# Optimization experiments

Measured on AMD Instinct MI355X. Metric: run time of the kernel, lower is better.

Reference implementation:

```python
import jax, jax.numpy as jnp
import numpy as np

D_MODEL = 1024
PATCH = 16
HID = 256
VOCAB = 256

def setup_inputs() -> dict:
    key = jax.random.key(0)
    ks = jax.random.split(key, 12)
    B, N = 16, 512
    s = lambda *sh: 1.0 / np.sqrt(sh[-1])
    inp = {
        'latents': jax.random.normal(ks[0], (B, N, D_MODEL), dtype=jnp.float32),
        'target_bytes': jax.random.randint(ks[1], (B, N * PATCH), 0, VOCAB, dtype=jnp.int64),
        'W_proj': jax.random.normal(ks[2], (HID, D_MODEL), dtype=jnp.float32) * s(HID, D_MODEL),
        'b_proj': jnp.zeros((HID,), dtype=jnp.float32),
        'emb_table': jax.random.normal(ks[3], (VOCAB, HID), dtype=jnp.float32),
        'W_ih': jax.random.normal(ks[4], (3 * HID, 2 * HID), dtype=jnp.float32) * s(1, 2 * HID),
        'W_hh': jax.random.normal(ks[5], (3 * HID, HID), dtype=jnp.float32) * s(1, HID),
        'b_ih': jnp.zeros((3 * HID,), dtype=jnp.float32),
        'b_hh': jnp.zeros((3 * HID,), dtype=jnp.float32),
        'W_head': jax.random.normal(ks[6], (VOCAB, HID), dtype=jnp.float32) * s(VOCAB, HID),
        'b_head': jnp.zeros((VOCAB,), dtype=jnp.float32),
    }
    return inp

def _gru_scan(x_proj, W_hh, b_hh, h0):
    # x_proj: [T, BN, 3H] precomputed input projections (incl. b_ih)
    def step(h, xg):
        hg = h @ W_hh.T + b_hh                      # [BN, 3H]
        xr, xz, xn = jnp.split(xg, 3, axis=-1)
        hr, hz, hn = jnp.split(hg, 3, axis=-1)
        r = jax.nn.sigmoid(xr + hr)
        z = jax.nn.sigmoid(xz + hz)
        n = jnp.tanh(xn + r * hn)
        h_new = (1.0 - z) * n + z * h
        return h_new, h_new
    _, outs = jax.lax.scan(step, h0, x_proj)
    return outs                                      # [T, BN, H]

def reference(latents, target_bytes, W_proj, b_proj, emb_table, W_ih, W_hh, b_ih, b_hh, W_head, b_head):
    B, N, D = latents.shape
    BN = B * N
    latent_ctx = (latents.reshape(BN, D) @ W_proj.T + b_proj)        # [BN, H]
    targets = target_bytes.reshape(BN, PATCH)
    sos = jnp.zeros((BN, 1), dtype=targets.dtype)
    rnn_in_bytes = jnp.concatenate([sos, targets[:, :-1]], axis=1)   # [BN, P]
    emb = emb_table[rnn_in_bytes]                                    # [BN, P, H]
    lat_exp = jnp.broadcast_to(latent_ctx[:, None, :], (BN, PATCH, HID))
    rnn_input = jnp.concatenate([emb, lat_exp], axis=-1)             # [BN, P, 2H]
    x_proj = jnp.einsum('bpi,gi->bpg', rnn_input, W_ih) + b_ih       # [BN, P, 3H]
    h0 = jnp.zeros((BN, HID), dtype=latents.dtype)
    outs = _gru_scan(jnp.swapaxes(x_proj, 0, 1), W_hh, b_hh, h0)     # [P, BN, H]
    outs = jnp.swapaxes(outs, 0, 1)                                  # [BN, P, H]
    logits = jnp.einsum('bph,vh->bpv', outs, W_head) + b_head        # [BN, P, 256]
    return logits.reshape(B, N, PATCH, VOCAB)
```

## Files before the change

kernel.cpp:

```cpp
#include <hip/hip_runtime.h>
#include <math.h>

#define NSEQ 8192
#define PATCHL 16
#define HIDN 256
#define VOCABN 256

typedef __attribute__((ext_vector_type(4))) float f32x4;
typedef __attribute__((ext_vector_type(8))) short bf16x8;

__device__ __forceinline__ unsigned short f2bf(float f) {
    unsigned int x = __float_as_uint(f);
    unsigned int r = (x + 0x7fffu + ((x >> 16) & 1u)) >> 16;
    return (unsigned short)r;
}
__device__ __forceinline__ float bf2f(unsigned short b) {
    return __uint_as_float(((unsigned int)b) << 16);
}
__device__ __forceinline__ float sigf(float x)   { return 1.f / (1.f + __expf(-x)); }
__device__ __forceinline__ float tanhf_(float x) { return 2.f / (1.f + __expf(-2.f * x)) - 1.f; }

__global__ __launch_bounds__(256)
void pack_frag(const float* __restrict__ src, int ld, int col0, int nks,
               unsigned short* __restrict__ dst)
{
    const int g = blockIdx.x * 256 + threadIdx.x;
    const int lane = g & 63;
    const int ks = (g / 64) % nks;
    const int T  = g / (64 * nks);
    const float* s = src + (size_t)(T * 16 + (lane & 15)) * ld + col0 + ks * 32 + ((lane >> 4) & 3) * 8;
    unsigned int q[4];
#pragma unroll
    for (int j = 0; j < 4; j++) {
        unsigned int lo = f2bf(s[2 * j]);
        unsigned int hi = f2bf(s[2 * j + 1]);
        q[j] = lo | (hi << 16);
    }
    uint4 v; v.x = q[0]; v.y = q[1]; v.z = q[2]; v.w = q[3];
    *(uint4*)(dst + (size_t)g * 8) = v;
}

template<bool ASRC_BF16, bool OUT_BF16>
__global__ __launch_bounds__(512)
void gemm_mfma(const void* __restrict__ Asrc, int lda,
               const unsigned short* __restrict__ bpack, int nks_total,
               const float* __restrict__ bias, void* __restrict__ Cdst, int ldc,
               int K)
{
    const int tid = threadIdx.x;
    const int w = tid >> 6, lane = tid & 63;
    const int l15 = lane & 15, kg = (lane >> 4) & 3;
    const int bm = blockIdx.x * 128, bn = blockIdx.y * 64;

    __shared__ unsigned short As[2][128 * 64];

    const int srow = tid >> 2;
    const int scol = (tid & 3) * 16;
    const int nkt = K / 64;

    f32x4 acc[4];
#pragma unroll
    for (int nt = 0; nt < 4; nt++) acc[nt] = 0.f;

    const int wb0 = srow * 128 + ((scol * 2) ^ ((srow & 7) << 4));
    const int wb1 = srow * 128 + ((scol * 2 + 16) ^ ((srow & 7) << 4));

#define STAGE(kt, buf) do {                                                         \
        const int gk = (kt) * 64 + scol;                                            \
        unsigned short tmp[16];                                                     \
        if (ASRC_BF16) {                                                            \
            const unsigned short* A = (const unsigned short*)Asrc;                  \
            *(uint4*)(tmp)     = *(const uint4*)(A + (size_t)(bm + srow) * lda + gk);      \
            *(uint4*)(tmp + 8) = *(const uint4*)(A + (size_t)(bm + srow) * lda + gk + 8);  \
        } else {                                                                    \
            const float* A = (const float*)Asrc;                                    \
            const float4 a0 = *(const float4*)(A + (size_t)(bm + srow) * lda + gk);       \
            const float4 a1 = *(const float4*)(A + (size_t)(bm + srow) * lda + gk + 4);   \
            const float4 a2 = *(const float4*)(A + (size_t)(bm + srow) * lda + gk + 8);   \
            const float4 a3 = *(const float4*)(A + (size_t)(bm + srow) * lda + gk + 12);  \
            tmp[0] = f2bf(a0.x);  tmp[1] = f2bf(a0.y);  tmp[2] = f2bf(a0.z);  tmp[3] = f2bf(a0.w);   \
            tmp[4] = f2bf(a1.x);  tmp[5] = f2bf(a1.y);  tmp[6] = f2bf(a1.z);  tmp[7] = f2bf(a1.w);   \
            tmp[8] = f2bf(a2.x);  tmp[9] = f2bf(a2.y);  tmp[10] = f2bf(a2.z); tmp[11] = f2bf(a2.w);  \
            tmp[12] = f2bf(a3.x); tmp[13] = f2bf(a3.y); tmp[14] = f2bf(a3.z); tmp[15] = f2bf(a3.w);  \
        }                                                                           \
        *(uint4*)((char*)As[buf] + wb0) = *(uint4*)tmp;                             \
        *(uint4*)((char*)As[buf] + wb1) = *(uint4*)(tmp + 8);                       \
    } while (0)

    STAGE(0, 0);
    __syncthreads();

    for (int kt = 0; kt < nkt; ++kt) {
        if (kt + 1 < nkt) STAGE(kt + 1, (kt + 1) & 1);
        const unsigned short* buf = As[kt & 1];
        const int row = w * 16 + l15;
#pragma unroll
        for (int ks = 0; ks < 2; ++ks) {
            const int bo = row * 128 + (((ks * 64) + kg * 16) ^ ((row & 7) << 4));
            const bf16x8 a = *(const bf16x8*)((const char*)buf + bo);
#pragma unroll
            for (int nt = 0; nt < 4; ++nt) {
                const int T = blockIdx.y * 4 + nt;
                const bf16x8 b = *(const bf16x8*)(bpack + (((size_t)T * nks_total + (kt * 2 + ks)) * 64 + lane) * 8);
                acc[nt] = __builtin_amdgcn_mfma_f32_16x16x32_bf16(a, b, acc[nt], 0, 0, 0);
            }
        }
        __syncthreads();
    }
#undef STAGE

#pragma unroll
    for (int nt = 0; nt < 4; ++nt) {
        const int n = bn + nt * 16 + l15;
        const float bv = bias ? bias[n] : 0.f;
#pragma unroll
        for (int rr = 0; rr < 4; ++rr) {
            const int m = bm + w * 16 + kg * 4 + rr;
            const float v = acc[nt][rr] + bv;
            if (OUT_BF16) ((unsigned short*)Cdst)[(size_t)m * ldc + n] = f2bf(v);
            else          ((float*)Cdst)[(size_t)m * ldc + n] = v;
        }
    }
}

#define PMS 776
__global__ __launch_bounds__(512)
void gru_scan_fused(const int* __restrict__ bytes,
                    const float* __restrict__ latg,
                    const unsigned short* __restrict__ premixB,
                    const unsigned short* __restrict__ wpack,
                    const float* __restrict__ b_hh,
                    unsigned short* __restrict__ hh,
                    int seq0)
{
    const int tid  = threadIdx.x;
    const int w    = tid >> 6;
    const int lane = tid & 63;
    const int l15  = lane & 15;
    const int kg   = (lane >> 4) & 3;
    const int s0l  = blockIdx.x * 32;
    const int s0g  = seq0 + s0l;

    __shared__ unsigned short PMs[32 * PMS];
    __shared__ unsigned short H[32 * 256];
    __shared__ int BYs[512];

    BYs[tid] = bytes[(size_t)s0g * PATCHL + tid];

    float bhr[2], bhz[2], bhn[2];
#pragma unroll
    for (int nt = 0; nt < 2; nt++) {
        const int u = w * 32 + nt * 16 + l15;
        bhr[nt] = b_hh[u]; bhz[nt] = b_hh[256 + u]; bhn[nt] = b_hh[512 + u];
    }

    float lgr[2][2][4], lgz[2][2][4], lgn[2][2][4];
#pragma unroll
    for (int mt = 0; mt < 2; mt++)
#pragma unroll
        for (int nt = 0; nt < 2; nt++) {
            const int u = w * 32 + nt * 16 + l15;
#pragma unroll
            for (int rr = 0; rr < 4; rr++) {
                const int sg = s0g + mt * 16 + kg * 4 + rr;
                const float* lg = latg + (size_t)sg * 768;
                lgr[mt][nt][rr] = lg[u]       + bhr[nt];
                lgz[mt][nt][rr] = lg[u + 256] + bhz[nt];
                lgn[mt][nt][rr] = lg[u + 512];
            }
        }

    float hreg[2][2][4];
#pragma unroll
    for (int mt = 0; mt < 2; mt++)
#pragma unroll
        for (int nt = 0; nt < 2; nt++)
#pragma unroll
            for (int rr = 0; rr < 4; rr++) hreg[mt][nt][rr] = 0.f;

    __syncthreads();

    for (int p = 0; p < PATCHL; ++p) {
#pragma unroll
        for (int j = 0; j < 6; ++j) {
            const int idx = j * 512 + tid;
            const int row = idx / 96, col = idx - row * 96;
            const int bv = p ? BYs[row * PATCHL + p - 1] : 0;
            *(uint4*)(PMs + row * PMS + col * 8) =
                *(const uint4*)(premixB + (size_t)bv * 768 + col * 8);
        }

        if (p) {
#pragma unroll
            for (int rj = 0; rj < 4; ++rj) {
                const int row = w * 4 + rj;
                const int boff = (lane * 8) ^ ((row & 7) << 4);
                const ushort4 v = *(const ushort4*)((const char*)(H + row * 256) + boff);
                *(ushort4*)(hh + ((size_t)(s0l + row) * PATCHL + (p - 1)) * 256 + lane * 4) = v;
            }
        }

        f32x4 accr[2][2], accz[2][2], accn[2][2];
#pragma unroll
        for (int mt = 0; mt < 2; mt++)
#pragma unroll
            for (int nt = 0; nt < 2; nt++) {
                accr[mt][nt] = 0.f; accz[mt][nt] = 0.f; accn[mt][nt] = 0.f;
            }
        if (p != 0) {
#pragma unroll
            for (int ks = 0; ks < 8; ++ks) {
                bf16x8 a[2];
#pragma unroll
                for (int mt = 0; mt < 2; mt++) {
                    const int s = mt * 16 + l15;
                    const int off = (ks * 64 + kg * 16) ^ ((s & 7) << 4);
                    a[mt] = *(const bf16x8*)(H + s * 256 + (off >> 1));
                }
#pragma unroll
                for (int nt = 0; nt < 2; nt++) {
                    const int tb = w * 2 + nt;
                    const bf16x8 br = *(const bf16x8*)(wpack + (((size_t)(tb)      * 8 + ks) * 64 + lane) * 8);
                    const bf16x8 bz = *(const bf16x8*)(wpack + (((size_t)(16 + tb) * 8 + ks) * 64 + lane) * 8);
                    const bf16x8 bn = *(const bf16x8*)(wpack + (((size_t)(32 + tb) * 8 + ks) * 64 + lane) * 8);
#pragma unroll
                    for (int mt = 0; mt < 2; mt++) {
                        accr[mt][nt] = __builtin_amdgcn_mfma_f32_16x16x32_bf16(a[mt], br, accr[mt][nt], 0, 0, 0);
                        accz[mt][nt] = __builtin_amdgcn_mfma_f32_16x16x32_bf16(a[mt], bz, accz[mt][nt], 0, 0, 0);
                        accn[mt][nt] = __builtin_amdgcn_mfma_f32_16x16x32_bf16(a[mt], bn, accn[mt][nt], 0, 0, 0);
                    }
                }
            }
        }
        __syncthreads();

#pragma unroll
        for (int mt = 0; mt < 2; mt++)
#pragma unroll
            for (int nt = 0; nt < 2; nt++) {
                const int u = w * 32 + nt * 16 + l15;
#pragma unroll
                for (int rr = 0; rr < 4; rr++) {
                    const int sl = mt * 16 + kg * 4 + rr;
                    const float xr = lgr[mt][nt][rr] + bf2f(PMs[sl * PMS + u]);
                    const float xz = lgz[mt][nt][rr] + bf2f(PMs[sl * PMS + 256 + u]);
                    const float xn = lgn[mt][nt][rr] + bf2f(PMs[sl * PMS + 512 + u]);
                    const float r = sigf(xr + accr[mt][nt][rr]);
                    const float z = sigf(xz + accz[mt][nt][rr]);
                    const float n = tanhf_(xn + r * (accn[mt][nt][rr] + bhn[nt]));
                    const float hn_ = (1.f - z) * n + z * hreg[mt][nt][rr];
                    hreg[mt][nt][rr] = hn_;
                    const int bo = (2 * u) ^ ((sl & 7) << 4);
                    H[sl * 256 + (bo >> 1)] = f2bf(hn_);
                }
            }
        __syncthreads();
    }

#pragma unroll
    for (int rj = 0; rj < 4; ++rj) {
        const int row = w * 4 + rj;
        const int boff = (lane * 8) ^ ((row & 7) << 4);
        const ushort4 v = *(const ushort4*)((const char*)(H + row * 256) + boff);
        *(ushort4*)(hh + ((size_t)(s0l + row) * PATCHL + (PATCHL - 1)) * 256 + lane * 4) = v;
    }
}

extern "C" void kernel_launch(void* const* d_in, const int* in_sizes, int n_in,
                              void* d_out, int out_size, void* d_ws, size_t ws_size,
                              hipStream_t stream)
{
    const float* latents = (const float*)d_in[0];
    const int*   tb      = (const int*)d_in[1];
    const float* W_proj  = (const float*)d_in[2];
    const float* b_proj  = (const float*)d_in[3];
    const float* emb     = (const float*)d_in[4];
    const float* W_ih    = (const float*)d_in[5];
    const float* W_hh    = (const float*)d_in[6];
    const float* b_ih    = (const float*)d_in[7];
    const float* b_hh    = (const float*)d_in[8];
    const float* W_head  = (const float*)d_in[9];
    const float* b_head  = (const float*)d_in[10];
    float* out = (float*)d_out;

    char* w = (char*)d_ws;
    float* latg = (float*)w;                               w += (size_t)NSEQ * 768 * 4;
    unsigned short* ctxb    = (unsigned short*)w;          w += (size_t)NSEQ * HIDN * 2;
    unsigned short* premixB = (unsigned short*)w;          w += 256 * 768 * 2;
    unsigned short* bpack1  = (unsigned short*)w;          w += 16 * 32 * 64 * 8 * 2;
    unsigned short* bpack2  = (unsigned short*)w;          w += 48 * 8 * 64 * 8 * 2;
    unsigned short* bpack3  = (unsigned short*)w;          w += 48 * 8 * 64 * 8 * 2;
    unsigned short* wpackG  = (unsigned short*)w;          w += 48 * 8 * 64 * 8 * 2;
    unsigned short* bpackH  = (unsigned short*)w;          w += 16 * 8 * 64 * 8 * 2;
    unsigned short* hh_c    = (unsigned short*)w;
    const size_t fixed_bytes = (size_t)(w - (char*)d_ws);
    const size_t chunk_full  = (size_t)NSEQ * PATCHL * 256 * 2;

    int nch = 1;
    while (nch < 16 && fixed_bytes + chunk_full / nch > ws_size) nch <<= 1;
    const int SPC = NSEQ / nch;

    hipLaunchKernelGGL(pack_frag, dim3(128), dim3(256), 0, stream, W_proj, 1024, 0, 32, bpack1);
    hipLaunchKernelGGL(pack_frag, dim3(96),  dim3(256), 0, stream, W_ih,   512, 256, 8, bpack2);
    hipLaunchKernelGGL(pack_frag, dim3(96),  dim3(256), 0, stream, W_ih,   512, 0,   8, bpack3);
    hipLaunchKernelGGL(pack_frag, dim3(96),  dim3(256), 0, stream, W_hh,   256, 0,   8, wpackG);
    hipLaunchKernelGGL(pack_frag, dim3(32),  dim3(256), 0, stream, W_head, 256, 0,   8, bpackH);

    hipLaunchKernelGGL((gemm_mfma<false, true>), dim3(2, 12), dim3(512), 0, stream,
                       emb, 256, bpack3, 8, nullptr, premixB, 768, 256);
    hipLaunchKernelGGL((gemm_mfma<false, true>), dim3(NSEQ / 128, 4), dim3(512), 0, stream,
                       latents, 1024, bpack1, 32, b_proj, ctxb, 256, 1024);
    hipLaunchKernelGGL((gemm_mfma<true, false>), dim3(NSEQ / 128, 12), dim3(512), 0, stream,
                       ctxb, 256, bpack2, 8, b_ih, latg, 768, 256);

    for (int c = 0; c < nch; ++c) {
        const int seq0 = c * SPC;
        hipLaunchKernelGGL(gru_scan_fused, dim3(SPC / 32), dim3(512), 0, stream,
                           tb, latg, premixB, wpackG, b_hh, hh_c, seq0);
        hipLaunchKernelGGL((gemm_mfma<true, false>), dim3(SPC * PATCHL / 128, 4), dim3(512), 0, stream,
                           hh_c, 256, bpackH, 8, b_head,
                           out + (size_t)seq0 * PATCHL * VOCABN, 256, 256);
    }
}
```

Before: 409.1 us.

## Interleave gate projections as bf16 quads and stage latent gates in LDS

The latent-gate projection is now stored as bf16 in a gate-interleaved layout (r,z,n,pad per hidden unit) instead of fp32 planar. The byte-embedding premix table uses the same layout. The scan kernel stages each block's latent gates into shared memory once and reads both tables with a single 8-byte load per unit, instead of holding 24 fp32 values per thread in registers. This cuts register pressure and the global bytes for latg, but adds about 66KB of LDS per block, which may lower occupancy. It also adds bf16 rounding of the latent gates and a padded fourth slot.

```diff
diff --git a/kernel.cpp b/kernel.cpp
--- a/kernel.cpp
+++ b/kernel.cpp
@@ -40,7 +40,7 @@
     *(uint4*)(dst + (size_t)g * 8) = v;
 }
 
-template<bool ASRC_BF16, bool OUT_BF16>
+template<bool ASRC_BF16, int OUT_MODE>
 __global__ __launch_bounds__(512)
 void gemm_mfma(const void* __restrict__ Asrc, int lda,
                const unsigned short* __restrict__ bpack, int nks_total,
@@ -117,17 +117,18 @@
         for (int rr = 0; rr < 4; ++rr) {
             const int m = bm + w * 16 + kg * 4 + rr;
             const float v = acc[nt][rr] + bv;
-            if (OUT_BF16) ((unsigned short*)Cdst)[(size_t)m * ldc + n] = f2bf(v);
-            else          ((float*)Cdst)[(size_t)m * ldc + n] = v;
-        }
-    }
-}
-
-#define PMS 776
+            if (OUT_MODE == 0)      ((float*)Cdst)[(size_t)m * ldc + n] = v;
+            else if (OUT_MODE == 1) ((unsigned short*)Cdst)[(size_t)m * ldc + n] = f2bf(v);
+            else                    ((unsigned short*)Cdst)[(size_t)m * 1024 + (n & 255) * 4 + (n >> 8)] = f2bf(v);
+        }
+    }
+}
+
+#define G4S 1032
 __global__ __launch_bounds__(512)
 void gru_scan_fused(const int* __restrict__ bytes,
-                    const float* __restrict__ latg,
-                    const unsigned short* __restrict__ premixB,
+                    const unsigned short* __restrict__ latg4,
+                    const unsigned short* __restrict__ pmx4,
                     const unsigned short* __restrict__ wpack,
                     const float* __restrict__ b_hh,
                     unsigned short* __restrict__ hh,
@@ -141,11 +142,20 @@
     const int s0l  = blockIdx.x * 32;
     const int s0g  = seq0 + s0l;
 
-    __shared__ unsigned short PMs[32 * PMS];
+    __shared__ unsigned short PMs[32 * G4S];
+    __shared__ unsigned short LG[32 * G4S];
     __shared__ unsigned short H[32 * 256];
     __shared__ int BYs[512];
 
     BYs[tid] = bytes[(size_t)s0g * PATCHL + tid];
+
+#pragma unroll
+    for (int j = 0; j < 8; ++j) {
+        const int idx = j * 512 + tid;
+        const int row = idx >> 7, col = idx & 127;
+        *(uint4*)(LG + row * G4S + col * 8) =
+            *(const uint4*)(latg4 + (size_t)(s0g + row) * 1024 + col * 8);
+    }
 
     float bhr[2], bhz[2], bhn[2];
 #pragma unroll
@@ -154,26 +164,10 @@
         bhr[nt] = b_hh[u]; bhz[nt] = b_hh[256 + u]; bhn[nt] = b_hh[512 + u];
     }
 
-    float lgr[2][2][4], lgz[2][2][4], lgn[2][2][4];
+    float hreg[2][2][4];
 #pragma unroll
     for (int mt = 0; mt < 2; mt++)
 #pragma unroll
-        for (int nt = 0; nt < 2; nt++) {
-            const int u = w * 32 + nt * 16 + l15;
-#pragma unroll
-            for (int rr = 0; rr < 4; rr++) {
-                const int sg = s0g + mt * 16 + kg * 4 + rr;
-                const float* lg = latg + (size_t)sg * 768;
-                lgr[mt][nt][rr] = lg[u]       + bhr[nt];
-                lgz[mt][nt][rr] = lg[u + 256] + bhz[nt];
-                lgn[mt][nt][rr] = lg[u + 512];
-            }
-        }
-
-    float hreg[2][2][4];
-#pragma unroll
-    for (int mt = 0; mt < 2; mt++)
-#pragma unroll
         for (int nt = 0; nt < 2; nt++)
 #pragma unroll
             for (int rr = 0; rr < 4; rr++) hreg[mt][nt][rr] = 0.f;
@@ -182,12 +176,12 @@
 
     for (int p = 0; p < PATCHL; ++p) {
 #pragma unroll
-        for (int j = 0; j < 6; ++j) {
+        for (int j = 0; j < 8; ++j) {
             const int idx = j * 512 + tid;
-            const int row = idx / 96, col = idx - row * 96;
+            const int row = idx >> 7, col = idx & 127;
             const int bv = p ? BYs[row * PATCHL + p - 1] : 0;
-            *(uint4*)(PMs + row * PMS + col * 8) =
-                *(const uint4*)(premixB + (size_t)bv * 768 + col * 8);
+            *(uint4*)(PMs + row * G4S + col * 8) =
+                *(const uint4*)(pmx4 + (size_t)bv * 1024 + col * 8);
         }
 
         if (p) {
@@ -242,9 +236,11 @@
 #pragma unroll
                 for (int rr = 0; rr < 4; rr++) {
                     const int sl = mt * 16 + kg * 4 + rr;
-                    const float xr = lgr[mt][nt][rr] + bf2f(PMs[sl * PMS + u]);
-                    const float xz = lgz[mt][nt][rr] + bf2f(PMs[sl * PMS + 256 + u]);
-                    const float xn = lgn[mt][nt][rr] + bf2f(PMs[sl * PMS + 512 + u]);
+                    const ushort4 pm4 = *(const ushort4*)(PMs + sl * G4S + u * 4);
+                    const ushort4 lg4 = *(const ushort4*)(LG  + sl * G4S + u * 4);
+                    const float xr = bf2f(lg4.x) + bf2f(pm4.x) + bhr[nt];
+                    const float xz = bf2f(lg4.y) + bf2f(pm4.y) + bhz[nt];
+                    const float xn = bf2f(lg4.z) + bf2f(pm4.z);
                     const float r = sigf(xr + accr[mt][nt][rr]);
                     const float z = sigf(xz + accz[mt][nt][rr]);
                     const float n = tanhf_(xn + r * (accn[mt][nt][rr] + bhn[nt]));
@@ -284,9 +280,9 @@
     float* out = (float*)d_out;
 
     char* w = (char*)d_ws;
-    float* latg = (float*)w;                               w += (size_t)NSEQ * 768 * 4;
+    unsigned short* latg4   = (unsigned short*)w;          w += (size_t)NSEQ * 1024 * 2;
     unsigned short* ctxb    = (unsigned short*)w;          w += (size_t)NSEQ * HIDN * 2;
-    unsigned short* premixB = (unsigned short*)w;          w += 256 * 768 * 2;
+    unsigned short* pmx4    = (unsigned short*)w;          w += 256 * 1024 * 2;
     unsigned short* bpack1  = (unsigned short*)w;          w += 16 * 32 * 64 * 8 * 2;
     unsigned short* bpack2  = (unsigned short*)w;          w += 48 * 8 * 64 * 8 * 2;
     unsigned short* bpack3  = (unsigned short*)w;          w += 48 * 8 * 64 * 8 * 2;
@@ -306,18 +302,18 @@
     hipLaunchKernelGGL(pack_frag, dim3(96),  dim3(256), 0, stream, W_hh,   256, 0,   8, wpackG);
     hipLaunchKernelGGL(pack_frag, dim3(32),  dim3(256), 0, stream, W_head, 256, 0,   8, bpackH);
 
-    hipLaunchKernelGGL((gemm_mfma<false, true>), dim3(2, 12), dim3(512), 0, stream,
-                       emb, 256, bpack3, 8, nullptr, premixB, 768, 256);
-    hipLaunchKernelGGL((gemm_mfma<false, true>), dim3(NSEQ / 128, 4), dim3(512), 0, stream,
+    hipLaunchKernelGGL((gemm_mfma<false, 2>), dim3(2, 12), dim3(512), 0, stream,
+                       emb, 256, bpack3, 8, nullptr, pmx4, 1024, 256);
+    hipLaunchKernelGGL((gemm_mfma<false, 1>), dim3(NSEQ / 128, 4), dim3(512), 0, stream,
                        latents, 1024, bpack1, 32, b_proj, ctxb, 256, 1024);
-    hipLaunchKernelGGL((gemm_mfma<true, false>), dim3(NSEQ / 128, 12), dim3(512), 0, stream,
-                       ctxb, 256, bpack2, 8, b_ih, latg, 768, 256);
+    hipLaunchKernelGGL((gemm_mfma<true, 2>), dim3(NSEQ / 128, 12), dim3(512), 0, stream,
+                       ctxb, 256, bpack2, 8, b_ih, latg4, 1024, 256);
 
     for (int c = 0; c < nch; ++c) {
         const int seq0 = c * SPC;
         hipLaunchKernelGGL(gru_scan_fused, dim3(SPC / 32), dim3(512), 0, stream,
-                           tb, latg, premixB, wpackG, b_hh, hh_c, seq0);
-        hipLaunchKernelGGL((gemm_mfma<true, false>), dim3(SPC * PATCHL / 128, 4), dim3(512), 0, stream,
+                           tb, latg4, pmx4, wpackG, b_hh, hh_c, seq0);
+        hipLaunchKernelGGL((gemm_mfma<true, 0>), dim3(SPC * PATCHL / 128, 4), dim3(512), 0, stream,
                            hh_c, 256, bpackH, 8, b_head,
                            out + (size_t)seq0 * PATCHL * VOCABN, 256, 256);
     }
```

Result: faster. 355.5 us (-13.1%).
